# Kernel optimization log

Measured on AMD Instinct MI355X. Metric: run time of the kernel, lower is better.

## Reference

```python
import jax, jax.numpy as jnp
import numpy as np

N_NODES = 50000
N_EDGES = 800000
D = 64          # node_in_feats == out_feats
N_STEPS = 3


def setup_inputs() -> dict:
    key = jax.random.key(0)
    ks = jax.random.split(key, 9)
    s = 1.0 / np.sqrt(D)
    return {
        "node_in": jax.random.normal(ks[0], (N_NODES, D), jnp.float32),
        # edge-type-0 linear (DGL GatedGraphConv self.linears[0])
        "W": jax.random.uniform(ks[1], (D, D), jnp.float32, -s, s),
        "b": jax.random.uniform(ks[2], (D,), jnp.float32, -s, s),
        # GRUCell params (torch layout: rows = [r, z, n] blocks)
        "Wih": jax.random.uniform(ks[3], (3 * D, D), jnp.float32, -s, s),
        "Whh": jax.random.uniform(ks[4], (3 * D, D), jnp.float32, -s, s),
        "bih": jax.random.uniform(ks[5], (3 * D,), jnp.float32, -s, s),
        "bhh": jax.random.uniform(ks[6], (3 * D,), jnp.float32, -s, s),
        "src": jax.random.randint(ks[7], (N_EDGES,), 0, N_NODES, jnp.int32),
        "dst": jax.random.randint(ks[8], (N_EDGES,), 0, N_NODES, jnp.int32),
    }


def _gru_cell(x, h, Wih, Whh, bih, bhh):
    gi = x @ Wih.T + bih   # [N, 3D]
    gh = h @ Whh.T + bhh   # [N, 3D]
    i_r, i_z, i_n = jnp.split(gi, 3, axis=-1)
    h_r, h_z, h_n = jnp.split(gh, 3, axis=-1)
    r = jax.nn.sigmoid(i_r + h_r)
    z = jax.nn.sigmoid(i_z + h_z)
    n = jnp.tanh(i_n + r * h_n)
    return (1.0 - z) * n + z * h


def reference(node_in, W, b, Wih, Whh, bih, bhh, src, dst):
    # DGL GatedGraphConv, n_steps=3, n_etypes=1. node_in_feats == out_feats,
    # so no zero-padding needed. The wrapper's tanh/dropout result is
    # discarded (h is overwritten by the second conv1 call), so the module
    # output is exactly one GatedGraphConv forward.
    h = node_in
    for _ in range(N_STEPS):
        wh = h @ W.T + b                                   # per-node transform; edge msg = wh[src]
        msg = wh[src]                                      # [E, D] gather
        a = jax.ops.segment_sum(msg, dst, num_segments=N_NODES)  # scatter-sum aggregation
        h = _gru_cell(a, h, Wih, Whh, bih, bhh)
    return h
```

## Files before the change

kernel.cpp:

```cpp
#include <hip/hip_runtime.h>

#define D 64
#define EXS 388
#define SGS 72
#define CHUNK 8192
#define PTH 512
#define MAXB 4096

typedef __bf16 bf16x8 __attribute__((ext_vector_type(8)));
typedef float f32x4 __attribute__((ext_vector_type(4)));

union U16 { uint4 u; bf16x8 b; };

__device__ __forceinline__ unsigned short f2bf(float f) {
    unsigned u = __float_as_uint(f);
    u += 0x7fff + ((u >> 16) & 1);
    return (unsigned short)(u >> 16);
}
__device__ __forceinline__ float bf2f(unsigned short s) {
    return __uint_as_float(((unsigned)s) << 16);
}


__global__ __launch_bounds__(256) void setup_kernel(const float* __restrict__ in,
                                                    unsigned short* __restrict__ hb0,
                                                    unsigned short* __restrict__ hb1,
                                                    const float* __restrict__ W,
                                                    const float* __restrict__ Wih,
                                                    const float* __restrict__ Whh,
                                                    const float* __restrict__ b,
                                                    unsigned short* __restrict__ Bpack,
                                                    float* __restrict__ cvec,
                                                    int* __restrict__ gcursor,
                                                    int n4, int nCvt, int N, int NBUK) {
    if ((int)blockIdx.x < nCvt) {
        int i = blockIdx.x * 256 + threadIdx.x;
        if (i < n4) {
            float4 v = ((const float4*)in)[i];
            ushort4 o;
            o.x = f2bf(v.x); o.y = f2bf(v.y); o.z = f2bf(v.z); o.w = f2bf(v.w);
            ((ushort4*)hb0)[i] = o;
        }
        if (blockIdx.x == 0) {
            if (threadIdx.x < 16) {
                ((ushort4*)(hb0 + (size_t)N * D))[threadIdx.x] = (ushort4){0, 0, 0, 0};
                ((ushort4*)(hb1 + (size_t)N * D))[threadIdx.x] = (ushort4){0, 0, 0, 0};
            }
            for (int j = threadIdx.x; j < NBUK; j += 256) gcursor[j] = 0;
        }
        return;
    }
    if (threadIdx.x >= 128) return;
    int blk = blockIdx.x - nCvt;
    int g = blk >> 2, t = blk & 3;
    int ks = threadIdx.x >> 6, lane = threadIdx.x & 63;
    int col = (g % 3) * 64 + t * 16 + (lane & 15);
    int kbase = ks * 32 + ((lane >> 4) & 3) * 8;
    size_t base = ((size_t)(blk * 2 + ks) * 64 + lane) * 8;
#pragma unroll
    for (int j = 0; j < 8; ++j) {
        int k = kbase + j;
        float v;
        if (g < 3) {
            v = 0.f;
#pragma unroll
            for (int m = 0; m < D; ++m) v += Wih[col * D + m] * W[m * D + k];
        } else {
            v = Whh[col * D + k];
        }
        Bpack[base + j] = f2bf(v);
    }
    if (g < 3 && ks == 0 && ((lane >> 4) & 3) == 0) {
        float acc = 0.f;
#pragma unroll
        for (int k = 0; k < D; ++k) acc += Wih[col * D + k] * b[k];
        cvec[col] = acc;
    }
}


__global__ __launch_bounds__(PTH) void partition_kernel(const int* __restrict__ src,
                                                        const int* __restrict__ dst,
                                                        int* __restrict__ gcursor,
                                                        unsigned* __restrict__ pairs,
                                                        int E, int NBUK) {
    __shared__ unsigned pl[CHUNK];
    __shared__ unsigned short bk[CHUNK];
    __shared__ int hist[512];
    __shared__ int scn[512];
    __shared__ int goff[512];
    int g = blockIdx.x;
    int t = threadIdx.x;
    int beg = g * CHUNK;
    int end = min(beg + CHUNK, E);
    int m = end - beg;
    hist[t] = 0;
    __syncthreads();
    for (int i = t; i < m; i += PTH)
        atomicAdd(&hist[dst[beg + i] >> 7], 1);
    __syncthreads();
    int own = hist[t];
    scn[t] = own;
    __syncthreads();
    for (int off = 1; off < 512; off <<= 1) {
        int cur = scn[t];
        int add = (t >= off) ? scn[t - off] : 0;
        __syncthreads();
        scn[t] = cur + add;
        __syncthreads();
    }
    int excl = scn[t] - own;
    hist[t] = excl;
    if (t < NBUK) {
        int gbase = own ? atomicAdd(&gcursor[t], own) : 0;
        goff[t] = t * MAXB + gbase - excl;
    }
    __syncthreads();
    for (int i = t; i < m; i += PTH) {
        int d = dst[beg + i];
        int s = src[beg + i];
        int b = d >> 7;
        int pos = atomicAdd(&hist[b], 1);
        pl[pos] = ((unsigned)s << 7) | (unsigned)(d & 127);
        bk[pos] = (unsigned short)b;
    }
    __syncthreads();
    for (int i = t; i < m; i += PTH)
        pairs[goff[bk[i]] + i] = pl[i];
}


__global__ __launch_bounds__(256) void bucket_sort_kernel(const unsigned* __restrict__ pairs,
                                                          const int* __restrict__ gcnt,
                                                          int* __restrict__ srcs_sorted,
                                                          int* __restrict__ row_beg,
                                                          int* __restrict__ row_end,
                                                          int NBUK, int N) {
    __shared__ unsigned pl[MAXB];
    __shared__ int srcl[MAXB];
    __shared__ int cnt[128];
    __shared__ int sc[128];
    __shared__ int cur2[128];
    int b = blockIdx.x;
    int t = threadIdx.x;
    int beg = b * MAXB;
    int m = gcnt[b];
    if (m > MAXB) m = MAXB;
    if (t < 128) cnt[t] = 0;
    __syncthreads();
    for (int i = t; i < m; i += 256) {
        unsigned p = pairs[beg + i];
        pl[i] = p;
        atomicAdd(&cnt[p & 127], 1);
    }
    __syncthreads();
    int vt = 0;
    if (t < 128) { vt = cnt[t]; sc[t] = vt; }
    __syncthreads();
    for (int off = 1; off < 128; off <<= 1) {
        int v2 = 0;
        if (t < 128) { v2 = sc[t] + ((t >= off) ? sc[t - off] : 0); }
        __syncthreads();
        if (t < 128) sc[t] = v2;
        __syncthreads();
    }
    int excl = (t < 128) ? (sc[t] - vt) : 0;
    if (t < 128) {
        int gid = b * 128 + t;
        if (gid < N) {
            row_beg[gid] = beg + excl;
            row_end[gid] = beg + excl + vt;
        }
        cur2[t] = excl;
    }
    __syncthreads();
    for (int i = t; i < m; i += 256) {
        unsigned p = pl[i];
        int r = atomicAdd(&cur2[p & 127], 1);
        srcl[r] = (int)(p >> 7);
    }
    __syncthreads();
    for (int i = t; i < m; i += 256) srcs_sorted[beg + i] = srcl[i];
}


__global__ __launch_bounds__(512) void fused2_kernel(const unsigned short* __restrict__ hb_in,
                                                     unsigned short* __restrict__ hb_out,
                                                     float* __restrict__ Fout, int writeF32,
                                                     const unsigned short* __restrict__ Bpack,
                                                     const float* __restrict__ cvec,
                                                     const float* __restrict__ bih,
                                                     const float* __restrict__ bhh,
                                                     const int* __restrict__ row_beg,
                                                     const int* __restrict__ row_end,
                                                     const int* __restrict__ srcs,
                                                     int N) {
    __shared__ unsigned short sg[16 * SGS];
    __shared__ float ex[16 * EXS];
    int tid = threadIdx.x;
    int g = tid >> 6;
    int lane = tid & 63;
    int base = blockIdx.x * 16;

    {
        int es = lane >> 3;
        int fo = lane & 7;
        int nlA = g, nlB = g + 8;
        int nodeA = base + nlA, nodeB = base + nlB;
        int begA = 0, endA = 0, begB = 0, endB = 0;
        if (nodeA < N) { begA = row_beg[nodeA]; endA = row_end[nodeA]; }
        if (nodeB < N) { begB = row_beg[nodeB]; endB = row_end[nodeB]; }

        int sA[4], sB[4];
#pragma unroll
        for (int j = 0; j < 4; ++j) {
            int eA = begA + 8 * j + es;
            int eB = begB + 8 * j + es;
            sA[j] = (eA < endA) ? srcs[eA] : N;
            sB[j] = (eB < endB) ? srcs[eB] : N;
        }
        uint4 dA[4], dB[4];
#pragma unroll
        for (int j = 0; j < 4; ++j) dA[j] = *(const uint4*)(hb_in + (size_t)sA[j] * D + fo * 8);
#pragma unroll
        for (int j = 0; j < 4; ++j) dB[j] = *(const uint4*)(hb_in + (size_t)sB[j] * D + fo * 8);

        float accA[8], accB[8];
#pragma unroll
        for (int j = 0; j < 8; ++j) { accA[j] = 0.f; accB[j] = 0.f; }
#pragma unroll
        for (int j = 0; j < 4; ++j) {
            unsigned ua[4] = {dA[j].x, dA[j].y, dA[j].z, dA[j].w};
            unsigned ub[4] = {dB[j].x, dB[j].y, dB[j].z, dB[j].w};
#pragma unroll
            for (int k = 0; k < 4; ++k) {
                accA[2 * k]     += bf2f((unsigned short)(ua[k] & 0xffff));
                accA[2 * k + 1] += bf2f((unsigned short)(ua[k] >> 16));
                accB[2 * k]     += bf2f((unsigned short)(ub[k] & 0xffff));
                accB[2 * k + 1] += bf2f((unsigned short)(ub[k] >> 16));
            }
        }
        for (int i = begA + 32; i < endA; i += 8) {
            int e = i + es;
            int s = (e < endA) ? srcs[e] : N;
            uint4 dd = *(const uint4*)(hb_in + (size_t)s * D + fo * 8);
            unsigned uu[4] = {dd.x, dd.y, dd.z, dd.w};
#pragma unroll
            for (int k = 0; k < 4; ++k) {
                accA[2 * k]     += bf2f((unsigned short)(uu[k] & 0xffff));
                accA[2 * k + 1] += bf2f((unsigned short)(uu[k] >> 16));
            }
        }
        for (int i = begB + 32; i < endB; i += 8) {
            int e = i + es;
            int s = (e < endB) ? srcs[e] : N;
            uint4 dd = *(const uint4*)(hb_in + (size_t)s * D + fo * 8);
            unsigned uu[4] = {dd.x, dd.y, dd.z, dd.w};
#pragma unroll
            for (int k = 0; k < 4; ++k) {
                accB[2 * k]     += bf2f((unsigned short)(uu[k] & 0xffff));
                accB[2 * k + 1] += bf2f((unsigned short)(uu[k] >> 16));
            }
        }
#pragma unroll
        for (int st = 8; st < 64; st <<= 1)
#pragma unroll
            for (int j = 0; j < 8; ++j) {
                accA[j] += __shfl_xor(accA[j], st, 64);
                accB[j] += __shfl_xor(accB[j], st, 64);
            }
        if (es == 0) {
            uint4 oA, oB;
            oA.x = (unsigned)f2bf(accA[0]) | ((unsigned)f2bf(accA[1]) << 16);
            oA.y = (unsigned)f2bf(accA[2]) | ((unsigned)f2bf(accA[3]) << 16);
            oA.z = (unsigned)f2bf(accA[4]) | ((unsigned)f2bf(accA[5]) << 16);
            oA.w = (unsigned)f2bf(accA[6]) | ((unsigned)f2bf(accA[7]) << 16);
            oB.x = (unsigned)f2bf(accB[0]) | ((unsigned)f2bf(accB[1]) << 16);
            oB.y = (unsigned)f2bf(accB[2]) | ((unsigned)f2bf(accB[3]) << 16);
            oB.z = (unsigned)f2bf(accB[4]) | ((unsigned)f2bf(accB[5]) << 16);
            oB.w = (unsigned)f2bf(accB[6]) | ((unsigned)f2bf(accB[7]) << 16);
            *(uint4*)(sg + nlA * SGS + fo * 8) = oA;
            *(uint4*)(sg + nlB * SGS + fo * 8) = oB;
        }
    }
    __syncthreads();

    if (g < 6) {
        int r16 = lane & 15, quad = lane >> 4;
        bf16x8 bf[4][2];
        const uint4* bp = (const uint4*)Bpack;
#pragma unroll
        for (int t = 0; t < 4; ++t)
#pragma unroll
            for (int ks = 0; ks < 2; ++ks) {
                U16 u; u.u = bp[((g * 4 + t) * 2 + ks) * 64 + lane];
                bf[t][ks] = u.b;
            }
        bf16x8 af[2];
        if (g < 3) {
#pragma unroll
            for (int ks = 0; ks < 2; ++ks) {
                U16 u; u.u = *(const uint4*)(sg + r16 * SGS + ks * 32 + quad * 8);
                af[ks] = u.b;
            }
        } else {
            int row = base + r16;
            if (row >= N) row = N - 1;
#pragma unroll
            for (int ks = 0; ks < 2; ++ks) {
                U16 u; u.u = *(const uint4*)(hb_in + (size_t)row * D + ks * 32 + quad * 8);
                af[ks] = u.b;
            }
        }
        f32x4 acc[4];
#pragma unroll
        for (int t = 0; t < 4; ++t) acc[t] = (f32x4){0.f, 0.f, 0.f, 0.f};
#pragma unroll
        for (int t = 0; t < 4; ++t)
#pragma unroll
            for (int ks = 0; ks < 2; ++ks)
                acc[t] = __builtin_amdgcn_mfma_f32_16x16x32_bf16(af[ks], bf[t][ks], acc[t], 0, 0, 0);
#pragma unroll
        for (int t = 0; t < 4; ++t)
#pragma unroll
            for (int r = 0; r < 4; ++r)
                ex[(quad * 4 + r) * EXS + g * 64 + t * 16 + r16] = acc[t][r];
    }
    __syncthreads();

    for (int idx = tid; idx < 16 * D; idx += 512) {
        int i = idx >> 6, d = idx & 63;
        int node = base + i;
        if (node < N) {
            const float* p = &ex[i * EXS];
            float deg = (float)(row_end[node] - row_beg[node]);
            float ir = p[d] + bih[d] + deg * cvec[d];
            float iz = p[64 + d] + bih[64 + d] + deg * cvec[64 + d];
            float in_ = p[128 + d] + bih[128 + d] + deg * cvec[128 + d];
            float hr = p[192 + d] + bhh[d];
            float hz = p[256 + d] + bhh[64 + d];
            float hn = p[320 + d] + bhh[128 + d];
            float h = bf2f(hb_in[(size_t)node * D + d]);
            float r = 1.f / (1.f + __expf(-(ir + hr)));
            float z = 1.f / (1.f + __expf(-(iz + hz)));
            float nn = tanhf(in_ + r * hn);
            float hnew = (1.f - z) * nn + z * h;
            if (writeF32) Fout[(size_t)node * D + d] = hnew;
            else hb_out[(size_t)node * D + d] = f2bf(hnew);
        }
    }
}

extern "C" void kernel_launch(void* const* d_in, const int* in_sizes, int n_in,
                              void* d_out, int out_size, void* d_ws, size_t ws_size,
                              hipStream_t stream) {
    const float* node_in = (const float*)d_in[0];
    const float* W       = (const float*)d_in[1];
    const float* b       = (const float*)d_in[2];
    const float* Wih     = (const float*)d_in[3];
    const float* Whh     = (const float*)d_in[4];
    const float* bih     = (const float*)d_in[5];
    const float* bhh     = (const float*)d_in[6];
    const int*   src     = (const int*)d_in[7];
    const int*   dst     = (const int*)d_in[8];
    const int N = in_sizes[0] / D;
    const int E = in_sizes[7];
    float* out = (float*)d_out;

    const int G = (E + CHUNK - 1) / CHUNK;
    const int NBUK = (N + 127) >> 7;

    char* ws = (char*)d_ws;
    size_t off = 0;
    auto alloc = [&](size_t bytes) -> void* {
        void* p = ws + off;
        off += (bytes + 255) & ~(size_t)255;
        return p;
    };
    unsigned short* hb0    = (unsigned short*)alloc((size_t)(N + 1) * D * 2);
    unsigned short* hb1    = (unsigned short*)alloc((size_t)(N + 1) * D * 2);
    int*   row_beg         = (int*)alloc((size_t)NBUK * 128 * sizeof(int));
    int*   row_end         = (int*)alloc((size_t)NBUK * 128 * sizeof(int));
    int*   srcs_sorted     = (int*)alloc((size_t)NBUK * MAXB * sizeof(int));
    unsigned* pairs        = (unsigned*)alloc((size_t)NBUK * MAXB * sizeof(unsigned));
    int*   gcursor         = (int*)alloc((size_t)NBUK * sizeof(int));
    unsigned short* Bpack  = (unsigned short*)alloc((size_t)6 * 4 * 2 * 64 * 8 * 2);
    float* cvec            = (float*)alloc((size_t)192 * sizeof(float));

    const int n4 = N * D / 4;
    const int nCvt = (n4 + 255) / 256;
    setup_kernel<<<nCvt + 24, 256, 0, stream>>>(node_in, hb0, hb1, W, Wih, Whh, b,
                                                Bpack, cvec, gcursor, n4, nCvt, N, NBUK);

    partition_kernel<<<G, PTH, 0, stream>>>(src, dst, gcursor, pairs, E, NBUK);
    bucket_sort_kernel<<<NBUK, 256, 0, stream>>>(pairs, gcursor, srcs_sorted,
                                                 row_beg, row_end, NBUK, N);

    const int grid = (N + 15) / 16;
    fused2_kernel<<<grid, 512, 0, stream>>>(hb0, hb1, out, 0, Bpack, cvec, bih, bhh,
                                            row_beg, row_end, srcs_sorted, N);
    fused2_kernel<<<grid, 512, 0, stream>>>(hb1, hb0, out, 0, Bpack, cvec, bih, bhh,
                                            row_beg, row_end, srcs_sorted, N);
    fused2_kernel<<<grid, 512, 0, stream>>>(hb0, hb1, out, 1, Bpack, cvec, bih, bhh,
                                            row_beg, row_end, srcs_sorted, N);
}
```

Measured before the change: 207.7 us.

## Merge edge partition into setup kernel and halve partition chunk size

Folds the edge-partition pass into the setup kernel as extra blocks, so the bf16 conversion, weight packing and partitioning share one launch. The bucket cursor is now zeroed with a memset beforehand, and the partition chunk is halved to create more blocks. Block size goes to 512 for setup and bucket sort. This removes one launch and its serial dependency, at the cost of more global cursor atomics and a larger shared-memory footprint on the conversion blocks.

```diff
diff --git a/kernel.cpp b/kernel.cpp
--- a/kernel.cpp
+++ b/kernel.cpp
@@ -3,7 +3,7 @@
 #define D 64
 #define EXS 388
 #define SGS 72
-#define CHUNK 8192
+#define CHUNK 4096
 #define PTH 512
 #define MAXB 4096
 
@@ -22,7 +22,7 @@
 }
 
 
-__global__ __launch_bounds__(256) void setup_kernel(const float* __restrict__ in,
+__global__ __launch_bounds__(PTH) void setup_kernel(const float* __restrict__ in,
                                                     unsigned short* __restrict__ hb0,
                                                     unsigned short* __restrict__ hb1,
                                                     const float* __restrict__ W,
@@ -31,106 +31,104 @@
                                                     const float* __restrict__ b,
                                                     unsigned short* __restrict__ Bpack,
                                                     float* __restrict__ cvec,
+                                                    const int* __restrict__ src,
+                                                    const int* __restrict__ dst,
                                                     int* __restrict__ gcursor,
-                                                    int n4, int nCvt, int N, int NBUK) {
+                                                    unsigned* __restrict__ pairs,
+                                                    int n4, int nCvt, int N, int NBUK, int E) {
+    __shared__ unsigned pl[CHUNK];
+    __shared__ unsigned short bk[CHUNK];
+    __shared__ int hist[512];
+    __shared__ int scn[512];
+    __shared__ int goff[512];
+
     if ((int)blockIdx.x < nCvt) {
-        int i = blockIdx.x * 256 + threadIdx.x;
+        int i = blockIdx.x * PTH + threadIdx.x;
         if (i < n4) {
             float4 v = ((const float4*)in)[i];
             ushort4 o;
             o.x = f2bf(v.x); o.y = f2bf(v.y); o.z = f2bf(v.z); o.w = f2bf(v.w);
             ((ushort4*)hb0)[i] = o;
         }
-        if (blockIdx.x == 0) {
-            if (threadIdx.x < 16) {
-                ((ushort4*)(hb0 + (size_t)N * D))[threadIdx.x] = (ushort4){0, 0, 0, 0};
-                ((ushort4*)(hb1 + (size_t)N * D))[threadIdx.x] = (ushort4){0, 0, 0, 0};
-            }
-            for (int j = threadIdx.x; j < NBUK; j += 256) gcursor[j] = 0;
+        if (blockIdx.x == 0 && threadIdx.x < 16) {
+            ((ushort4*)(hb0 + (size_t)N * D))[threadIdx.x] = (ushort4){0, 0, 0, 0};
+            ((ushort4*)(hb1 + (size_t)N * D))[threadIdx.x] = (ushort4){0, 0, 0, 0};
         }
         return;
     }
-    if (threadIdx.x >= 128) return;
     int blk = blockIdx.x - nCvt;
-    int g = blk >> 2, t = blk & 3;
-    int ks = threadIdx.x >> 6, lane = threadIdx.x & 63;
-    int col = (g % 3) * 64 + t * 16 + (lane & 15);
-    int kbase = ks * 32 + ((lane >> 4) & 3) * 8;
-    size_t base = ((size_t)(blk * 2 + ks) * 64 + lane) * 8;
-#pragma unroll
-    for (int j = 0; j < 8; ++j) {
-        int k = kbase + j;
-        float v;
-        if (g < 3) {
-            v = 0.f;
-#pragma unroll
-            for (int m = 0; m < D; ++m) v += Wih[col * D + m] * W[m * D + k];
-        } else {
-            v = Whh[col * D + k];
-        }
-        Bpack[base + j] = f2bf(v);
-    }
-    if (g < 3 && ks == 0 && ((lane >> 4) & 3) == 0) {
-        float acc = 0.f;
-#pragma unroll
-        for (int k = 0; k < D; ++k) acc += Wih[col * D + k] * b[k];
-        cvec[col] = acc;
-    }
-}
-
-
-__global__ __launch_bounds__(PTH) void partition_kernel(const int* __restrict__ src,
-                                                        const int* __restrict__ dst,
-                                                        int* __restrict__ gcursor,
-                                                        unsigned* __restrict__ pairs,
-                                                        int E, int NBUK) {
-    __shared__ unsigned pl[CHUNK];
-    __shared__ unsigned short bk[CHUNK];
-    __shared__ int hist[512];
-    __shared__ int scn[512];
-    __shared__ int goff[512];
-    int g = blockIdx.x;
-    int t = threadIdx.x;
-    int beg = g * CHUNK;
-    int end = min(beg + CHUNK, E);
-    int m = end - beg;
-    hist[t] = 0;
-    __syncthreads();
-    for (int i = t; i < m; i += PTH)
-        atomicAdd(&hist[dst[beg + i] >> 7], 1);
-    __syncthreads();
-    int own = hist[t];
-    scn[t] = own;
-    __syncthreads();
-    for (int off = 1; off < 512; off <<= 1) {
-        int cur = scn[t];
-        int add = (t >= off) ? scn[t - off] : 0;
-        __syncthreads();
-        scn[t] = cur + add;
-        __syncthreads();
-    }
-    int excl = scn[t] - own;
-    hist[t] = excl;
-    if (t < NBUK) {
-        int gbase = own ? atomicAdd(&gcursor[t], own) : 0;
-        goff[t] = t * MAXB + gbase - excl;
-    }
-    __syncthreads();
-    for (int i = t; i < m; i += PTH) {
-        int d = dst[beg + i];
-        int s = src[beg + i];
-        int b = d >> 7;
-        int pos = atomicAdd(&hist[b], 1);
-        pl[pos] = ((unsigned)s << 7) | (unsigned)(d & 127);
-        bk[pos] = (unsigned short)b;
-    }
-    __syncthreads();
-    for (int i = t; i < m; i += PTH)
-        pairs[goff[bk[i]] + i] = pl[i];
-}
-
-
-__global__ __launch_bounds__(256) void bucket_sort_kernel(const unsigned* __restrict__ pairs,
+    if (blk < 24) {
+        if (threadIdx.x >= 128) return;
+        int g = blk >> 2, t = blk & 3;
+        int ks = threadIdx.x >> 6, lane = threadIdx.x & 63;
+        int col = (g % 3) * 64 + t * 16 + (lane & 15);
+        int kbase = ks * 32 + ((lane >> 4) & 3) * 8;
+        size_t base = ((size_t)(blk * 2 + ks) * 64 + lane) * 8;
+#pragma unroll
+        for (int j = 0; j < 8; ++j) {
+            int k = kbase + j;
+            float v;
+            if (g < 3) {
+                v = 0.f;
+#pragma unroll
+                for (int m = 0; m < D; ++m) v += Wih[col * D + m] * W[m * D + k];
+            } else {
+                v = Whh[col * D + k];
+            }
+            Bpack[base + j] = f2bf(v);
+        }
+        if (g < 3 && ks == 0 && ((lane >> 4) & 3) == 0) {
+            float acc = 0.f;
+#pragma unroll
+            for (int k = 0; k < D; ++k) acc += Wih[col * D + k] * b[k];
+            cvec[col] = acc;
+        }
+        return;
+    }
+    {
+        int g = blk - 24;
+        int t = threadIdx.x;
+        int beg = g * CHUNK;
+        int end = min(beg + CHUNK, E);
+        int m = end - beg;
+        hist[t] = 0;
+        __syncthreads();
+        for (int i = t; i < m; i += PTH)
+            atomicAdd(&hist[dst[beg + i] >> 7], 1);
+        __syncthreads();
+        int own = hist[t];
+        scn[t] = own;
+        __syncthreads();
+        for (int off = 1; off < 512; off <<= 1) {
+            int cur = scn[t];
+            int add = (t >= off) ? scn[t - off] : 0;
+            __syncthreads();
+            scn[t] = cur + add;
+            __syncthreads();
+        }
+        int excl = scn[t] - own;
+        hist[t] = excl;
+        if (t < NBUK) {
+            int gbase = own ? atomicAdd(&gcursor[t], own) : 0;
+            goff[t] = t * MAXB + gbase - excl;
+        }
+        __syncthreads();
+        for (int i = t; i < m; i += PTH) {
+            int d = dst[beg + i];
+            int s = src[beg + i];
+            int bb = d >> 7;
+            int pos = atomicAdd(&hist[bb], 1);
+            pl[pos] = ((unsigned)s << 7) | (unsigned)(d & 127);
+            bk[pos] = (unsigned short)bb;
+        }
+        __syncthreads();
+        for (int i = t; i < m; i += PTH)
+            pairs[goff[bk[i]] + i] = pl[i];
+    }
+}
+
+
+__global__ __launch_bounds__(512) void bucket_sort_kernel(const unsigned* __restrict__ pairs,
                                                           const int* __restrict__ gcnt,
                                                           int* __restrict__ srcs_sorted,
                                                           int* __restrict__ row_beg,
@@ -148,7 +146,7 @@
     if (m > MAXB) m = MAXB;
     if (t < 128) cnt[t] = 0;
     __syncthreads();
-    for (int i = t; i < m; i += 256) {
+    for (int i = t; i < m; i += 512) {
         unsigned p = pairs[beg + i];
         pl[i] = p;
         atomicAdd(&cnt[p & 127], 1);
@@ -174,13 +172,13 @@
         cur2[t] = excl;
     }
     __syncthreads();
-    for (int i = t; i < m; i += 256) {
+    for (int i = t; i < m; i += 512) {
         unsigned p = pl[i];
         int r = atomicAdd(&cur2[p & 127], 1);
         srcl[r] = (int)(p >> 7);
     }
     __syncthreads();
-    for (int i = t; i < m; i += 256) srcs_sorted[beg + i] = srcl[i];
+    for (int i = t; i < m; i += 512) srcs_sorted[beg + i] = srcl[i];
 }
 
 
@@ -387,13 +385,15 @@
     unsigned short* Bpack  = (unsigned short*)alloc((size_t)6 * 4 * 2 * 64 * 8 * 2);
     float* cvec            = (float*)alloc((size_t)192 * sizeof(float));
 
+    hipMemsetAsync(gcursor, 0, (size_t)NBUK * sizeof(int), stream);
+
     const int n4 = N * D / 4;
-    const int nCvt = (n4 + 255) / 256;
-    setup_kernel<<<nCvt + 24, 256, 0, stream>>>(node_in, hb0, hb1, W, Wih, Whh, b,
-                                                Bpack, cvec, gcursor, n4, nCvt, N, NBUK);
-
-    partition_kernel<<<G, PTH, 0, stream>>>(src, dst, gcursor, pairs, E, NBUK);
-    bucket_sort_kernel<<<NBUK, 256, 0, stream>>>(pairs, gcursor, srcs_sorted,
+    const int nCvt = (n4 + PTH - 1) / PTH;
+    setup_kernel<<<nCvt + 24 + G, PTH, 0, stream>>>(node_in, hb0, hb1, W, Wih, Whh, b,
+                                                    Bpack, cvec, src, dst, gcursor, pairs,
+                                                    n4, nCvt, N, NBUK, E);
+
+    bucket_sort_kernel<<<NBUK, 512, 0, stream>>>(pairs, gcursor, srcs_sorted,
                                                  row_beg, row_end, NBUK, N);
 
     const int grid = (N + 15) / 16;
```

Result: faster. 201.5 us (-3.0%).
